# Optimization experiments

Measured on AMD Instinct MI355X. Metric: run time of the kernel, lower is better.

## Reference

```python
import jax, jax.numpy as jnp
import numpy as np

B, L, H, S = 32, 1024, 768, 16  # batch, seq len, hidden (bert-base), candidate segments


def setup_inputs() -> dict:
    rng = np.random.default_rng(0)
    # ragged valid lengths in [L/2, L]
    valid = rng.integers(L // 2, L + 1, size=B)
    attention_mask = (np.arange(L)[None, :] < valid[:, None]).astype(np.int32)
    # bos_locations[i][0] is the history length; S segment starts strictly increasing,
    # last segment ends at valid[i]
    bos = np.zeros((B, S), np.int32)
    for i in range(B):
        hist = int(valid[i]) // 4
        bos[i] = np.linspace(hist, int(valid[i]), S + 1)[:-1].astype(np.int32)
    key = jax.random.key(0)
    k1, k2 = jax.random.split(key)
    tokens = jax.random.normal(k1, (B, L, H), jnp.float32)
    fc_w = jax.random.normal(k2, (H,), jnp.float32) * 0.02
    fc_b = jnp.zeros((1,), jnp.float32)
    return {
        "tokens": tokens,
        "attention_mask": jnp.asarray(attention_mask),
        "bos_locations": jnp.asarray(bos),
        "fc_w": fc_w,
        "fc_b": fc_b,
    }


def reference(tokens, attention_mask, bos_locations, fc_w, fc_b):
    Bs, Ls, Hs = tokens.shape
    pos = jnp.arange(Ls)
    valid = attention_mask.sum(-1)  # [B] valid lengths

    def per_sample(v, bos, toks):
        hist = bos[0]
        # segment id of each position (−1 before first bos)
        seg = jnp.searchsorted(bos, pos, side="right") - 1  # [L]
        inv = pos < v  # [L] valid positions
        # arrow mask: inside valid region, attend if either side is in the history
        # prefix or both positions fall in the same bos-delimited segment
        mask = (
            inv[:, None]
            & inv[None, :]
            & ((pos[:, None] < hist) | (pos[None, :] < hist) | (seg[:, None] == seg[None, :]))
        ).astype(jnp.int32)  # [L, L]
        # segment-mean pooling via 0/1 indicator matmul (as in the original)
        ends = jnp.concatenate([bos[1:], v[None].astype(bos.dtype)])
        ind = ((pos[None, :] >= bos[:, None]) & (pos[None, :] < ends[:, None])).astype(toks.dtype)  # [S, L]
        mean = (ind @ toks) / ind.sum(-1, keepdims=True)  # [S, H]
        return mask, mean

    cand_attn_mask, mean_reps = jax.vmap(per_sample)(valid, bos_locations, tokens)
    mean_logits = jnp.einsum("bsh,h->bs", mean_reps, fc_w) + fc_b[0]  # squeeze(fc(.))
    return mean_logits, cand_attn_mask
```

## Files before the change

kernel.cpp:

```cpp
#include <hip/hip_runtime.h>

#define Bz 32
#define Lz 1024
#define Hz 768
#define Sz 16

typedef float f32x4 __attribute__((ext_vector_type(4)));

__device__ __forceinline__ int wave_valid(const int* __restrict__ amaskRow, int lane) {
  const int4* am4 = (const int4*)amaskRow;
  int s = 0;
#pragma unroll
  for (int j = 0; j < 4; ++j) {
    int4 a = am4[lane + j * 64];
    s += a.x + a.y + a.z + a.w;
  }
#pragma unroll
  for (int off = 32; off > 0; off >>= 1) s += __shfl_xor(s, off);
  return s;
}

__global__ __launch_bounds__(256) void fused_mask_dot(
    const float* __restrict__ tokens, const int* __restrict__ amask,
    const int* __restrict__ bos, const float* __restrict__ fc_w,
    float* __restrict__ maskOut, float* __restrict__ t) {
  int b = blockIdx.x >> 6;
  int local = blockIdx.x & 63;
  int wave = threadIdx.x >> 6;
  int lane = threadIdx.x & 63;

  int v = wave_valid(amask + b * Lz, lane);
  const int* bosRow = bos + b * Sz;
  int h = bosRow[0];

  const f32x4* wp = (const f32x4*)fc_w;
  f32x4 w0 = wp[lane];
  f32x4 w1 = wp[lane + 64];
  f32x4 w2 = wp[lane + 128];

#pragma unroll
  for (int it = 0; it < 4; ++it) {
    int q = local + ((it << 2) + wave) * 64;
    bool doDot = (q >= h && q < v);

    const f32x4* tp = (const f32x4*)(tokens + ((size_t)(b * Lz + q)) * Hz);
    f32x4 x0, x1, x2;
    if (doDot) {
      x0 = tp[lane];
      x1 = tp[lane + 64];
      x2 = tp[lane + 128];
    }

    int A, s0, s1;
    if (q >= v) { A = 0; s0 = 0; s1 = 0; }
    else if (q < h) { A = v; s0 = 0; s1 = 0; }
    else {
      int idx = -1;
#pragma unroll
      for (int s = 0; s < Sz; ++s) idx += (q >= bosRow[s]) ? 1 : 0;
      A = h;
      s0 = bosRow[idx];
      s1 = (idx < Sz - 1) ? bosRow[idx + 1] : v;
    }
    unsigned span = (unsigned)(s1 - s0);

    f32x4* row = (f32x4*)(maskOut + ((size_t)(b * Lz + q)) * Lz);
#pragma unroll
    for (int j = 0; j < 4; ++j) {
      int p0 = (lane + j * 64) * 4;
      f32x4 val;
      val.x = (p0 + 0 < A || (unsigned)(p0 + 0 - s0) < span) ? 1.f : 0.f;
      val.y = (p0 + 1 < A || (unsigned)(p0 + 1 - s0) < span) ? 1.f : 0.f;
      val.z = (p0 + 2 < A || (unsigned)(p0 + 2 - s0) < span) ? 1.f : 0.f;
      val.w = (p0 + 3 < A || (unsigned)(p0 + 3 - s0) < span) ? 1.f : 0.f;
      row[lane + j * 64] = val;
    }

    if (doDot) {
      float sum = x0.x * w0.x + x0.y * w0.y + x0.z * w0.z + x0.w * w0.w;
      sum += x1.x * w1.x + x1.y * w1.y + x1.z * w1.z + x1.w * w1.w;
      sum += x2.x * w2.x + x2.y * w2.y + x2.z * w2.z + x2.w * w2.w;
#pragma unroll
      for (int off = 32; off > 0; off >>= 1) sum += __shfl_down(sum, off);
      if (lane == 0) t[b * Lz + q] = sum;
    }
  }
}

__global__ __launch_bounds__(1024) void logits_kernel(
    const float* __restrict__ t, const int* __restrict__ bos,
    const int* __restrict__ amask, const float* __restrict__ fc_b,
    float* __restrict__ logits) {
  int b = blockIdx.x;
  int s = threadIdx.x >> 6;
  int lane = threadIdx.x & 63;

  int v = wave_valid(amask + b * Lz, lane);
  int beg = bos[b * Sz + s];
  int end = (s < Sz - 1) ? bos[b * Sz + s + 1] : v;

  float sum = 0.f;
  for (int p = beg + lane; p < end; p += 64) sum += t[b * Lz + p];
#pragma unroll
  for (int off = 32; off > 0; off >>= 1) sum += __shfl_down(sum, off);
  if (lane == 0) logits[b * Sz + s] = sum / (float)(end - beg) + fc_b[0];
}

extern "C" void kernel_launch(void* const* d_in, const int* in_sizes, int n_in,
                              void* d_out, int out_size, void* d_ws, size_t ws_size,
                              hipStream_t stream) {
  const float* tokens = (const float*)d_in[0];
  const int* amask = (const int*)d_in[1];
  const int* bos = (const int*)d_in[2];
  const float* fc_w = (const float*)d_in[3];
  const float* fc_b = (const float*)d_in[4];

  float* out = (float*)d_out;
  float* logits = out;
  float* maskOut = out + Bz * Sz;

  float* t = (float*)d_ws;

  fused_mask_dot<<<Bz * 64, 256, 0, stream>>>(tokens, amask, bos, fc_w, maskOut, t);
  logits_kernel<<<Bz, 1024, 0, stream>>>(t, bos, amask, fc_b, logits);
}
```

Baseline: 35.37 us.

## Fuse segment-mean logits into mask/dot kernel via atomic accumulation

```diff
diff --git a/kernel.cpp b/kernel.cpp
--- a/kernel.cpp
+++ b/kernel.cpp
@@ -20,10 +20,11 @@
   return s;
 }
 
-__global__ __launch_bounds__(256) void fused_mask_dot(
+__global__ __launch_bounds__(256) void fused_all(
     const float* __restrict__ tokens, const int* __restrict__ amask,
     const int* __restrict__ bos, const float* __restrict__ fc_w,
-    float* __restrict__ maskOut, float* __restrict__ t) {
+    const float* __restrict__ fc_b, float* __restrict__ maskOut,
+    float* __restrict__ logits) {
   int b = blockIdx.x >> 6;
   int local = blockIdx.x & 63;
   int wave = threadIdx.x >> 6;
@@ -32,6 +33,10 @@
   int v = wave_valid(amask + b * Lz, lane);
   const int* bosRow = bos + b * Sz;
   int h = bosRow[0];
+
+  if (local == 0 && threadIdx.x < Sz) {
+    atomicAdd(&logits[b * Sz + threadIdx.x], fc_b[0]);
+  }
 
   const f32x4* wp = (const f32x4*)fc_w;
   f32x4 w0 = wp[lane];
@@ -51,11 +56,11 @@
       x2 = tp[lane + 128];
     }
 
-    int A, s0, s1;
+    int A, s0, s1, idx = 0;
     if (q >= v) { A = 0; s0 = 0; s1 = 0; }
     else if (q < h) { A = v; s0 = 0; s1 = 0; }
     else {
-      int idx = -1;
+      idx = -1;
 #pragma unroll
       for (int s = 0; s < Sz; ++s) idx += (q >= bosRow[s]) ? 1 : 0;
       A = h;
@@ -82,28 +87,9 @@
       sum += x2.x * w2.x + x2.y * w2.y + x2.z * w2.z + x2.w * w2.w;
 #pragma unroll
       for (int off = 32; off > 0; off >>= 1) sum += __shfl_down(sum, off);
-      if (lane == 0) t[b * Lz + q] = sum;
+      if (lane == 0) atomicAdd(&logits[b * Sz + idx], sum / (float)span);
     }
   }
-}
-
-__global__ __launch_bounds__(1024) void logits_kernel(
-    const float* __restrict__ t, const int* __restrict__ bos,
-    const int* __restrict__ amask, const float* __restrict__ fc_b,
-    float* __restrict__ logits) {
-  int b = blockIdx.x;
-  int s = threadIdx.x >> 6;
-  int lane = threadIdx.x & 63;
-
-  int v = wave_valid(amask + b * Lz, lane);
-  int beg = bos[b * Sz + s];
-  int end = (s < Sz - 1) ? bos[b * Sz + s + 1] : v;
-
-  float sum = 0.f;
-  for (int p = beg + lane; p < end; p += 64) sum += t[b * Lz + p];
-#pragma unroll
-  for (int off = 32; off > 0; off >>= 1) sum += __shfl_down(sum, off);
-  if (lane == 0) logits[b * Sz + s] = sum / (float)(end - beg) + fc_b[0];
 }
 
 extern "C" void kernel_launch(void* const* d_in, const int* in_sizes, int n_in,
@@ -119,8 +105,7 @@
   float* logits = out;
   float* maskOut = out + Bz * Sz;
 
-  float* t = (float*)d_ws;
-
-  fused_mask_dot<<<Bz * 64, 256, 0, stream>>>(tokens, amask, bos, fc_w, maskOut, t);
-  logits_kernel<<<Bz, 1024, 0, stream>>>(t, bos, amask, fc_b, logits);
+  hipMemsetAsync(logits, 0, Bz * Sz * sizeof(float), stream);
+  fused_all<<<Bz * 64, 256, 0, stream>>>(tokens, amask, bos, fc_w, fc_b,
+                                         maskOut, logits);
 }
```

New measurement: 50.85 us. +43.8%, slower.
